# Optimization experiments

Hardware: AMD Instinct MI355X
Metric: run time of the kernel (lower is better)

The kernel has to match this reference:

```python
import jax, jax.numpy as jnp
import numpy as np

EMBED_DIM = 1024
BATCH = 4
SEQ = 2048


def setup_inputs() -> dict:
    key = jax.random.key(0)
    ks = jax.random.split(key, 9)
    D = EMBED_DIM
    s = 1.0 / np.sqrt(D)
    inputs = jax.random.normal(ks[0], (BATCH, SEQ, D), dtype=jnp.float32)
    rotation_params = jax.random.normal(ks[1], (D, D), dtype=jnp.float32) * s
    entangle_params = jax.random.normal(ks[2], (D, D), dtype=jnp.float32) * s
    Wq = jax.random.normal(ks[3], (D, D), dtype=jnp.float32) * s
    bq = jax.random.normal(ks[4], (D,), dtype=jnp.float32) * 0.01
    Wk = jax.random.normal(ks[5], (D, D), dtype=jnp.float32) * s
    bk = jax.random.normal(ks[6], (D,), dtype=jnp.float32) * 0.01
    Wv = jax.random.normal(ks[7], (D, D), dtype=jnp.float32) * s
    bv = jax.random.normal(ks[8], (D,), dtype=jnp.float32) * 0.01
    # causal mask: True = masked out (matches torch masked_fill semantics)
    mask = jnp.triu(jnp.ones((SEQ, SEQ), dtype=bool), k=1)
    return {"inputs": inputs, "rotation_params": rotation_params,
            "entangle_params": entangle_params, "Wq": Wq, "bq": bq,
            "Wk": Wk, "bk": bk, "Wv": Wv, "bv": bv, "mask": mask}


def reference(inputs, rotation_params, entangle_params, Wq, bq, Wk, bk, Wv, bv, mask):
    D = inputs.shape[-1]
    # q = Linear(x) @ R^T ; k = Linear(x) @ E^T ; v = Linear(x)
    q = (jnp.einsum('bsd,ed->bse', inputs, Wq) + bq) @ rotation_params.T
    k = (jnp.einsum('bsd,ed->bse', inputs, Wk) + bk) @ entangle_params.T
    v = jnp.einsum('bsd,ed->bse', inputs, Wv) + bv
    scores = jnp.einsum('bqd,bkd->bqk', q, k) / jnp.sqrt(jnp.float32(D))
    scores = jnp.where(mask, jnp.float32(-jnp.inf), scores)
    probs = jax.nn.softmax(scores, axis=-1)  # dropout=0.0 -> identity
    return jnp.einsum('bqk,bkd->bqd', probs, v)
```

## Files before the change

### kernel.cpp

```cpp
#include <hip/hip_runtime.h>
#include <hip/hip_bf16.h>
#include <stdint.h>
#include <math.h>

#define DD 1024
#define SS 2048
#define BB 4

typedef __bf16 bf16;
typedef __bf16 bf16x8 __attribute__((ext_vector_type(8)));
typedef __bf16 bf16x4 __attribute__((ext_vector_type(4)));
typedef float f32x4 __attribute__((ext_vector_type(4)));

__device__ __forceinline__ void gload_lds16(const bf16* g, bf16* l) {
  __builtin_amdgcn_global_load_lds(
      (const __attribute__((address_space(1))) void*)g,
      (__attribute__((address_space(3))) void*)l, 16, 0, 0);
}

__global__ __launch_bounds__(256) void prep_all(
    const float* __restrict__ x, const float* __restrict__ R,
    const float* __restrict__ E, const float* __restrict__ Wv,
    const float* __restrict__ Wq, const float* __restrict__ Wk,
    const float* __restrict__ bq, const float* __restrict__ bk,
    const float* __restrict__ bv, bf16* __restrict__ xb,
    bf16* __restrict__ Rb, bf16* __restrict__ Eb, bf16* __restrict__ Wvb,
    bf16* __restrict__ WqT, bf16* __restrict__ WkT, float* __restrict__ bias,
    float* __restrict__ rowsums) {
  int bid = blockIdx.x;
  int t = threadIdx.x;
  if (bid < 11264) {
    const float* src;
    bf16* dst;
    int base;
    if (bid < 8192) { src = x; dst = xb; base = bid; }
    else if (bid < 9216) { src = R; dst = Rb; base = bid - 8192; }
    else if (bid < 10240) { src = E; dst = Eb; base = bid - 9216; }
    else { src = Wv; dst = Wvb; base = bid - 10240; }
    int i = (base * 256 + t) * 4;
    float4 v = *(const float4*)(src + i);
    bf16x4 o;
    o.x = (bf16)v.x; o.y = (bf16)v.y; o.z = (bf16)v.z; o.w = (bf16)v.w;
    *(bf16x4*)(dst + i) = o;
  } else if (bid < 13312) {
    int r2 = bid - 11264;
    const float* src = (r2 >= 1024) ? Wk : Wq;
    bf16* dst = (r2 >= 1024) ? WkT : WqT;
    int rem = r2 & 1023;
    int bx = rem & 31, by = rem >> 5;
    __shared__ float tile[32][33];
    int tx = t & 31, ty = t >> 5;
    int xcol = bx * 32 + tx;
    int y0 = by * 32;
    for (int r = ty; r < 32; r += 8)
      tile[r][tx] = src[(y0 + r) * DD + xcol];
    __syncthreads();
    int dx = by * 32 + tx;
    int dy0 = bx * 32;
    for (int r = ty; r < 32; r += 8)
      dst[(dy0 + r) * DD + dx] = (bf16)tile[tx][r];
  } else if (bid < 16384) {
    int e = bid - 13312;
    if (e >= 2048) { if (t == 0) bias[e] = bv[e - 2048]; return; }
    const float* M = (e < 1024) ? R : E;
    const float* bb = (e < 1024) ? bq : bk;
    int row = e & 1023;
    float s = 0.f;
    for (int f = t; f < DD; f += 256) s += M[row * DD + f] * bb[f];
    for (int o = 32; o >= 1; o >>= 1) s += __shfl_xor(s, o, 64);
    __shared__ float red[4];
    if ((t & 63) == 0) red[t >> 6] = s;
    __syncthreads();
    if (t == 0) bias[e] = red[0] + red[1] + red[2] + red[3];
  } else {
    int idx = (bid - 16384) * 256 + t;
    rowsums[idx] = 0.f;
  }
}

#define QSTGA(pa, kt)                                                        \
  gload_lds16(A + (long)(w * 16 + srow) * DD + (kt) * 32 + scg,              \
              As + (pa) * 4096 + w * 512)
#define QSTGB(pb, h, kt)                                                     \
  gload_lds16(B + (long)((h) * 128 + w * 16 + srow) * DD + (kt) * 32 + scg,  \
              Bs + (pb) * 8192 + (h) * 4096 + w * 512)

#define QTILE(pa, pb, pa1, pb2, kA, kB, DOA, DOB, WAITN)                     \
  {                                                                          \
    bf16x8 af[4], bfr[4];                                                    \
    _Pragma("unroll") for (int i_ = 0; i_ < 4; i_++)                         \
        af[i_] = *(const bf16x8*)(a_base + (pa) * 4096 + i_ * 512);          \
    _Pragma("unroll") for (int j_ = 0; j_ < 4; j_++)                         \
        bfr[j_] = *(const bf16x8*)(b_base + (pb) * 8192 + j_ * 512);         \
    if (DOA) { QSTGA(pa1, kA); }                                             \
    if (DOB) { QSTGB(pb2, 0, kB); QSTGB(pb2, 1, kB); }                       \
    __builtin_amdgcn_s_barrier();                                            \
    asm volatile("s_waitcnt lgkmcnt(0)" ::: "memory");                       \
    __builtin_amdgcn_sched_barrier(0);                                       \
    __builtin_amdgcn_s_setprio(1);                                           \
    _Pragma("unroll") for (int i_ = 0; i_ < 4; i_++)                         \
        _Pragma("unroll") for (int j_ = 0; j_ < 4; j_++) acc[i_][j_] =       \
        __builtin_amdgcn_mfma_f32_16x16x32_bf16(af[i_], bfr[j_],             \
                                                acc[i_][j_], 0, 0, 0);       \
    __builtin_amdgcn_s_setprio(0);                                           \
    __builtin_amdgcn_sched_barrier(0);                                       \
    if ((WAITN) == 2) asm volatile("s_waitcnt vmcnt(2)" ::: "memory");       \
    if ((WAITN) == 0) asm volatile("s_waitcnt vmcnt(0)" ::: "memory");       \
    __builtin_amdgcn_s_barrier();                                            \
    __builtin_amdgcn_sched_barrier(0);                                       \
  }

#define QPROLOGUE_AND_LOOP                                                   \
  QSTGA(0, 0);                                                               \
  QSTGB(0, 0, 0); QSTGB(0, 1, 0);                                            \
  QSTGB(1, 0, 1); QSTGB(1, 1, 1);                                            \
  asm volatile("s_waitcnt vmcnt(2)" ::: "memory");                           \
  __builtin_amdgcn_s_barrier();                                              \
  __builtin_amdgcn_sched_barrier(0);                                         \
  _Pragma("unroll 1") for (int t6 = 0; t6 < 30; t6 += 6) {                   \
    QTILE(0, 0, 1, 2, t6 + 1, t6 + 2, 1, 1, 2)                               \
    QTILE(1, 1, 0, 0, t6 + 2, t6 + 3, 1, 1, 2)                               \
    QTILE(0, 2, 1, 1, t6 + 3, t6 + 4, 1, 1, 2)                               \
    QTILE(1, 0, 0, 2, t6 + 4, t6 + 5, 1, 1, 2)                               \
    QTILE(0, 1, 1, 0, t6 + 5, t6 + 6, 1, 1, 2)                               \
    QTILE(1, 2, 0, 1, t6 + 6, t6 + 7, 1, 1, 2)                               \
  }                                                                          \
  QTILE(0, 0, 1, 0, 31, 0, 1, 0, 0)     \
  QTILE(1, 1, 0, 0, 0, 0, 0, 0, -1)

__global__ __launch_bounds__(512, 4) void gemm_qkv(
    const bf16* __restrict__ Ag, const bf16* __restrict__ Bg,
    bf16* __restrict__ Cg, const float* __restrict__ bias,
    bf16* __restrict__ vTp) {
  __shared__ __align__(16) bf16 smem[32768];
  bf16* As = smem;
  bf16* Bs = smem + 8192;

  int id = (int)blockIdx.y * 12 + (int)blockIdx.x;
  int wg = (id & 7) * 96 + (id >> 3);
  int ck = wg / 96, r96 = wg % 96;
  int bx = (ck & 3) * 3 + r96 % 3;
  int by = (ck >> 2) * 32 + r96 / 3;
  long m0 = (long)by * 128, n0 = (long)bx * 256;
  const bf16* A = Ag + m0 * DD;
  const bf16* B = Bg + n0 * DD;

  int t = threadIdx.x;
  int w = t >> 6, l = t & 63;
  int wm = w >> 2, wn = w & 3;
  int ln = l & 15, quad = l >> 4;

  int srow = l >> 2;
  int scg = ((l & 3) ^ ((l >> 3) & 3)) * 8;
  int rdslot = (quad ^ ((ln >> 1) & 3)) * 8;
  const bf16* a_base = As + (wm * 64 + ln) * 32 + rdslot;
  const bf16* b_base = Bs + (wn * 64 + ln) * 32 + rdslot;

  f32x4 acc[4][4];
#pragma unroll
  for (int i = 0; i < 4; i++)
#pragma unroll
    for (int j = 0; j < 4; j++) acc[i][j] = f32x4{0.f, 0.f, 0.f, 0.f};

  QPROLOGUE_AND_LOOP

  __syncthreads();

  if (n0 < 2048) {
    bf16* C = Cg + m0 * 3072 + n0;
#pragma unroll
    for (int i = 0; i < 4; i++) {
      int rb = wm * 64 + i * 16 + quad * 4;
#pragma unroll
      for (int j = 0; j < 4; j++) {
        int col = wn * 64 + j * 16 + ln;
        float bv_ = bias[n0 + col];
#pragma unroll
        for (int r = 0; r < 4; r++)
          C[(long)(rb + r) * 3072 + col] = (bf16)(acc[i][j][r] + bv_);
      }
    }
  } else {
    int d0 = (int)n0 - 2048;
    int b = (int)(m0 >> 11);
    int s0 = (int)(m0 & 2047);
#pragma unroll
    for (int i = 0; i < 4; i++) {
      int sl = wm * 64 + i * 16 + quad * 4;
#pragma unroll
      for (int j = 0; j < 4; j++) {
        int d = wn * 64 + j * 16 + ln;
        float bv_ = bias[n0 + d];
#pragma unroll
        for (int r = 0; r < 4; r++)
          smem[d * 128 + ((sl + r) ^ ((d & 7) << 3))] =
              (bf16)(acc[i][j][r] + bv_);
      }
    }
    __syncthreads();
    int d = t >> 1, sh = t & 1;
    bf16* dst = vTp + (long)b * DD * SS + (long)(d0 + d) * SS + s0 + sh * 64;
#pragma unroll
    for (int c = 0; c < 8; ++c) {
      int sc = (sh * 64 + c * 8) ^ ((d & 7) << 3);
      *(bf16x8*)(dst + c * 8) = *(const bf16x8*)(smem + d * 128 + sc);
    }
  }
}

#define CSTGA(pa, kt)                                                        \
  gload_lds16(Aq + (long)(w * 16 + srow) * 3072 + (kt) * 32 + scg,           \
              As + (pa) * 4096 + w * 512)
#define CSTGB(pb, h, kt)                                                     \
  gload_lds16(Bk + (long)((h) * 128 + w * 16 + srow) * 3072 + (kt) * 32 +    \
                  scg,                                                       \
              Bs + (pb) * 8192 + (h) * 4096 + w * 512)

#define CTILE(pa, pb, pa1, pb2, kA, kB, DOA, DOB, WAITN)                     \
  {                                                                          \
    bf16x8 af[4], bfr[4];                                                    \
    _Pragma("unroll") for (int i_ = 0; i_ < 4; i_++)                         \
        af[i_] = *(const bf16x8*)(a_base + (pa) * 4096 + i_ * 512);          \
    _Pragma("unroll") for (int j_ = 0; j_ < 4; j_++)                         \
        bfr[j_] = *(const bf16x8*)(b_base + (pb) * 8192 + j_ * 512);         \
    if (DOA) { CSTGA(pa1, kA); }                                             \
    if (DOB) { CSTGB(pb2, 0, kB); CSTGB(pb2, 1, kB); }                       \
    __builtin_amdgcn_s_barrier();                                            \
    asm volatile("s_waitcnt lgkmcnt(0)" ::: "memory");                       \
    __builtin_amdgcn_sched_barrier(0);                                       \
    __builtin_amdgcn_s_setprio(1);                                           \
    _Pragma("unroll") for (int i_ = 0; i_ < 4; i_++)                         \
        _Pragma("unroll") for (int j_ = 0; j_ < 4; j_++) acc[i_][j_] =       \
        __builtin_amdgcn_mfma_f32_16x16x32_bf16(af[i_], bfr[j_],             \
                                                acc[i_][j_], 0, 0, 0);       \
    __builtin_amdgcn_s_setprio(0);                                           \
    __builtin_amdgcn_sched_barrier(0);                                       \
    if ((WAITN) == 2) asm volatile("s_waitcnt vmcnt(2)" ::: "memory");       \
    if ((WAITN) == 0) asm volatile("s_waitcnt vmcnt(0)" ::: "memory");       \
    __builtin_amdgcn_s_barrier();                                            \
    __builtin_amdgcn_sched_barrier(0);                                       \
  }

__global__ __launch_bounds__(512, 4) void scores256(
    const bf16* __restrict__ qkvp, bf16* __restrict__ P,
    float* __restrict__ rowsums) {
  __shared__ __align__(16) bf16 smem[32768];
  bf16* As = smem;
  bf16* Bs = smem + 8192;

  int bz = blockIdx.z;
  int id = (int)blockIdx.x;
  int q = (id & 7) * 9 + (id >> 3);
  int s = (int)sqrtf((float)q + 0.5f);
  while (s * s > q) s--;
  while ((s + 1) * (s + 1) <= q) s++;
  int by, bxc;
  if (q >= s * (s + 1)) { by = 2 * s; bxc = q - s * (s + 1); }
  else { by = 2 * s - 1; bxc = q - s * s; }
  long m0 = (long)by * 128, n0 = (long)bxc * 256;
  const bf16* Aq = qkvp + (long)bz * SS * 3072 + m0 * 3072;
  const bf16* Bk = qkvp + 1024 + (long)bz * SS * 3072 + n0 * 3072;

  int t = threadIdx.x;
  int w = t >> 6, l = t & 63;
  int wm = w >> 2, wn = w & 3;
  int ln = l & 15, quad = l >> 4;

  int srow = l >> 2;
  int scg = ((l & 3) ^ ((l >> 3) & 3)) * 8;
  int rdslot = (quad ^ ((ln >> 1) & 3)) * 8;
  const bf16* a_base = As + (wm * 64 + ln) * 32 + rdslot;
  const bf16* b_base = Bs + (wn * 64 + ln) * 32 + rdslot;

  f32x4 acc[4][4];
#pragma unroll
  for (int i = 0; i < 4; i++)
#pragma unroll
    for (int j = 0; j < 4; j++) acc[i][j] = f32x4{0.f, 0.f, 0.f, 0.f};

  CSTGA(0, 0);
  CSTGB(0, 0, 0); CSTGB(0, 1, 0);
  CSTGB(1, 0, 1); CSTGB(1, 1, 1);
  asm volatile("s_waitcnt vmcnt(2)" ::: "memory");
  __builtin_amdgcn_s_barrier();
  __builtin_amdgcn_sched_barrier(0);
#pragma unroll 1
  for (int t6 = 0; t6 < 30; t6 += 6) {
    CTILE(0, 0, 1, 2, t6 + 1, t6 + 2, 1, 1, 2)
    CTILE(1, 1, 0, 0, t6 + 2, t6 + 3, 1, 1, 2)
    CTILE(0, 2, 1, 1, t6 + 3, t6 + 4, 1, 1, 2)
    CTILE(1, 0, 0, 2, t6 + 4, t6 + 5, 1, 1, 2)
    CTILE(0, 1, 1, 0, t6 + 5, t6 + 6, 1, 1, 2)
    CTILE(1, 2, 0, 1, t6 + 6, t6 + 7, 1, 1, 2)
  }
  CTILE(0, 0, 1, 0, 31, 0, 1, 0, 0)
  CTILE(1, 1, 0, 0, 0, 0, 0, 0, -1)

  __syncthreads();

#pragma unroll
  for (int i = 0; i < 4; i++) {
    int rb = wm * 64 + i * 16 + quad * 4;
#pragma unroll
    for (int j = 0; j < 4; j++) {
      int col = wn * 64 + j * 16 + ln;
#pragma unroll
      for (int r = 0; r < 4; r++) {
        int row = rb + r;
        float p = 0.f;
        if (n0 + col <= m0 + row) p = __expf(acc[i][j][r] * 0.03125f);
        smem[row * 256 + (col ^ ((row & 7) << 3))] = (bf16)p;
      }
    }
  }
  __syncthreads();
  int row = t >> 2, qtr = t & 3;
  bf16* Pr = P + (long)bz * SS * SS + (m0 + row) * SS + n0;
  float rsum = 0.f;
#pragma unroll
  for (int c8 = 0; c8 < 8; c8++) {
    int p8 = qtr * 8 + c8;
    int slot = p8 ^ (row & 7);
    bf16x8 v = *(const bf16x8*)(smem + row * 256 + slot * 8);
#pragma unroll
    for (int e = 0; e < 8; e++) rsum += (float)v[e];
    *(bf16x8*)(Pr + p8 * 8) = v;
  }
  rsum += __shfl_xor(rsum, 1, 64);
  rsum += __shfl_xor(rsum, 2, 64);
  if (qtr == 0) atomicAdd(&rowsums[(long)bz * SS + m0 + row], rsum);
}

template <int MODE>
__global__ __launch_bounds__(256, 4)
void gemm_bt(const bf16* __restrict__ Ag, long lda, long sAb,
             const bf16* __restrict__ Bg, long ldb, long sBb,
             void* __restrict__ Cg, long ldc, long sCb,
             const float* __restrict__ bias, float scale, int K,
             bf16* __restrict__ vTp, float* __restrict__ rowsums) {
  __shared__ __align__(16) bf16 smem[16384];
  bf16* As = smem;
  bf16* Bs = smem + 8192;

  int bx = blockIdx.x, by = blockIdx.y, bz = blockIdx.z;
  if (MODE == 0) {
    int nx = (int)gridDim.x;
    int nwg = nx * (int)gridDim.y;
    int id = by * nx + bx;
    int xcd = id & 7, rest = id >> 3;
    int q8 = nwg >> 3, r8 = nwg & 7;
    int wg = (xcd < r8 ? xcd * (q8 + 1) : r8 * (q8 + 1) + (xcd - r8) * q8)
             + rest;
    bx = wg % nx;
    by = wg / nx;
  }
  if (MODE == 2) by = 15 - by;
  long m0 = (long)by * 128, n0 = (long)bx * 128;
  const bf16* A = Ag + (long)bz * sAb + m0 * lda;
  const bf16* Bp = Bg + (long)bz * sBb + n0 * ldb;

  int t = threadIdx.x;
  int w = t >> 6, l = t & 63;
  int lr = l >> 2;
  int lc = (((l & 3) ^ (lr & 3)) * 8);
  int quad = l >> 4, ln = l & 15;
  int wm = w >> 1, wn = w & 1;
  int rdoff = ((quad ^ (ln & 3)) * 8);

  int Keff = (MODE == 2) ? (by + 1) * 128 : K;

  f32x4 acc[4][4];
#pragma unroll
  for (int i = 0; i < 4; i++)
#pragma unroll
    for (int j = 0; j < 4; j++) acc[i][j] = f32x4{0.f, 0.f, 0.f, 0.f};

  const bf16* a_base = As + (wm * 64 + ln) * 32 + rdoff;
  const bf16* b_base = Bs + (wn * 64 + ln) * 32 + rdoff;
  long arow0 = (long)(w * 16 + lr);

#define STG(p, kc0)                                                         \
  {                                                                         \
    int kc = (kc0) + lc;                                                    \
    gload_lds16(A + arow0 * lda + kc, As + (p) * 4096 + w * 512);           \
    gload_lds16(A + (arow0 + 64) * lda + kc,                                \
                As + (p) * 4096 + 2048 + w * 512);                          \
    gload_lds16(Bp + arow0 * ldb + kc, Bs + (p) * 4096 + w * 512);          \
    gload_lds16(Bp + (arow0 + 64) * ldb + kc,                               \
                Bs + (p) * 4096 + 2048 + w * 512);                          \
  }

  STG(0, 0);
  int cur = 0;
  for (int k = 0; k < Keff; k += 32) {
    asm volatile("s_waitcnt vmcnt(0)" ::: "memory");
    __builtin_amdgcn_s_barrier();
    __builtin_amdgcn_sched_barrier(0);
    if (k + 32 < Keff) STG(cur ^ 1, k + 32);
    bf16x8 af[4], bfr[4];
#pragma unroll
    for (int i = 0; i < 4; i++) {
      af[i] = *(const bf16x8*)(a_base + cur * 4096 + i * 512);
      bfr[i] = *(const bf16x8*)(b_base + cur * 4096 + i * 512);
    }
#pragma unroll
    for (int i = 0; i < 4; i++)
#pragma unroll
      for (int j = 0; j < 4; j++)
        acc[i][j] = __builtin_amdgcn_mfma_f32_16x16x32_bf16(
            af[i], bfr[j], acc[i][j], 0, 0, 0);
    cur ^= 1;
  }
#undef STG
  __syncthreads();

  if (MODE == 0) {
    bf16* C = (bf16*)Cg + (long)bz * sCb + m0 * ldc + n0;
#pragma unroll
    for (int i = 0; i < 4; i++) {
      int rb = wm * 64 + i * 16 + quad * 4;
#pragma unroll
      for (int j = 0; j < 4; j++) {
        int col = wn * 64 + j * 16 + ln;
        float bv_ = bias ? bias[n0 + col] : 0.f;
#pragma unroll
        for (int r = 0; r < 4; r++)
          C[(long)(rb + r) * ldc + col] = (bf16)(acc[i][j][r] + bv_);
      }
    }
  } else {
    float* C = (float*)Cg + (long)bz * sCb + m0 * ldc + n0;
    const float* rs = rowsums + (long)bz * SS + m0;
#pragma unroll
    for (int i = 0; i < 4; i++) {
      int rb = wm * 64 + i * 16 + quad * 4;
      float inv[4];
#pragma unroll
      for (int r = 0; r < 4; r++) inv[r] = 1.f / rs[rb + r];
#pragma unroll
      for (int j = 0; j < 4; j++) {
        int col = wn * 64 + j * 16 + ln;
#pragma unroll
        for (int r = 0; r < 4; r++)
          C[(long)(rb + r) * ldc + col] = acc[i][j][r] * inv[r];
      }
    }
  }
}

extern "C" void kernel_launch(void* const* d_in, const int* in_sizes, int n_in,
                              void* d_out, int out_size, void* d_ws,
                              size_t ws_size, hipStream_t stream) {
  const float* x = (const float*)d_in[0];
  const float* R = (const float*)d_in[1];
  const float* E = (const float*)d_in[2];
  const float* Wq = (const float*)d_in[3];
  const float* bq = (const float*)d_in[4];
  const float* Wk = (const float*)d_in[5];
  const float* bk = (const float*)d_in[6];
  const float* Wv = (const float*)d_in[7];
  const float* bv = (const float*)d_in[8];
  float* out = (float*)d_out;

  char* ws = (char*)d_ws;
  bf16* qkv = (bf16*)ws;
  bf16* vT = (bf16*)(ws + 50331648);
  bf16* probs = (bf16*)(ws + 67108864);
  float* rowsums = (float*)(ws + 100663296);
  char* sr = ws + 101711872;
  bf16* xb = (bf16*)sr;
  bf16* Rb = (bf16*)(sr + 16777216);
  bf16* Eb = Rb + 1024 * 1024;
  bf16* WqT = (bf16*)(sr + 20971520);
  bf16* WkT = WqT + 1024 * 1024;
  bf16* wcat = (bf16*)(sr + 25165824);
  float* bias = (float*)(sr + 31457280);

  prep_all<<<16416, 256, 0, stream>>>(x, R, E, Wv, Wq, Wk, bq, bk, bv, xb, Rb,
                                      Eb, wcat + 2048 * DD, WqT, WkT, bias,
                                      rowsums);

  gemm_bt<0><<<dim3(8, 8, 2), 256, 0, stream>>>(
      Rb, DD, 1024 * 1024, WqT, DD, 1024 * 1024, wcat, DD, 1024 * 1024,
      nullptr, 1.f, DD, nullptr, nullptr);

  gemm_qkv<<<dim3(12, 64, 1), 512, 0, stream>>>(xb, wcat, qkv, bias, vT);

  scores256<<<dim3(72, 1, BB), 512, 0, stream>>>(qkv, probs, rowsums);

  gemm_bt<2><<<dim3(8, 16, BB), 256, 0, stream>>>(
      probs, SS, (long)SS * SS, vT, SS, (long)DD * SS, out,
      DD, (long)SS * DD, nullptr, 1.f, SS, nullptr, rowsums);
}
```

Baseline: 290.6 us.

## Replace QKV GEMM with 256x256 tile, 8-phase pipelined kernel using 128KB LDS

Rewrites the fused QKV projection GEMM so each workgroup computes a 256x256 tile instead of 128x256, with BK=64 double-buffered in 128KB of dynamic LDS. The main loop is split into eight MFMA phases that interleave global-to-LDS staging with compute, and the block-to-tile mapping is adjusted for the new grid. The aim is to cut global/LDS traffic per FLOP through larger tile reuse. In exchange, occupancy drops to 2 blocks per CU and register pressure rises with 32 accumulators per wave. The grid becomes 384 tiles, which may leave some CUs with uneven load.

```diff
diff --git a/kernel.cpp b/kernel.cpp
--- a/kernel.cpp
+++ b/kernel.cpp
@@ -78,70 +78,91 @@
   }
 }
 
-#define QSTGA(pa, kt)                                                        \
-  gload_lds16(A + (long)(w * 16 + srow) * DD + (kt) * 32 + scg,              \
-              As + (pa) * 4096 + w * 512)
-#define QSTGB(pb, h, kt)                                                     \
-  gload_lds16(B + (long)((h) * 128 + w * 16 + srow) * DD + (kt) * 32 + scg,  \
-              Bs + (pb) * 8192 + (h) * 4096 + w * 512)
-
-#define QTILE(pa, pb, pa1, pb2, kA, kB, DOA, DOB, WAITN)                     \
+#define AHTO(buf, h) ((buf) * 16384 + (h) * 8192)
+#define BHTO(buf, h) (32768 + (buf) * 16384 + (h) * 8192)
+
+#define STG_A(buf, h, kt)                                                    \
   {                                                                          \
-    bf16x8 af[4], bfr[4];                                                    \
-    _Pragma("unroll") for (int i_ = 0; i_ < 4; i_++)                         \
-        af[i_] = *(const bf16x8*)(a_base + (pa) * 4096 + i_ * 512);          \
-    _Pragma("unroll") for (int j_ = 0; j_ < 4; j_++)                         \
-        bfr[j_] = *(const bf16x8*)(b_base + (pb) * 8192 + j_ * 512);         \
-    if (DOA) { QSTGA(pa1, kA); }                                             \
-    if (DOB) { QSTGB(pb2, 0, kB); QSTGB(pb2, 1, kB); }                       \
-    __builtin_amdgcn_s_barrier();                                            \
-    asm volatile("s_waitcnt lgkmcnt(0)" ::: "memory");                       \
-    __builtin_amdgcn_sched_barrier(0);                                       \
-    __builtin_amdgcn_s_setprio(1);                                           \
-    _Pragma("unroll") for (int i_ = 0; i_ < 4; i_++)                         \
-        _Pragma("unroll") for (int j_ = 0; j_ < 4; j_++) acc[i_][j_] =       \
-        __builtin_amdgcn_mfma_f32_16x16x32_bf16(af[i_], bfr[j_],             \
-                                                acc[i_][j_], 0, 0, 0);       \
-    __builtin_amdgcn_s_setprio(0);                                           \
-    __builtin_amdgcn_sched_barrier(0);                                       \
-    if ((WAITN) == 2) asm volatile("s_waitcnt vmcnt(2)" ::: "memory");       \
-    if ((WAITN) == 0) asm volatile("s_waitcnt vmcnt(0)" ::: "memory");       \
-    __builtin_amdgcn_s_barrier();                                            \
-    __builtin_amdgcn_sched_barrier(0);                                       \
-  }
-
-#define QPROLOGUE_AND_LOOP                                                   \
-  QSTGA(0, 0);                                                               \
-  QSTGB(0, 0, 0); QSTGB(0, 1, 0);                                            \
-  QSTGB(1, 0, 1); QSTGB(1, 1, 1);                                            \
-  asm volatile("s_waitcnt vmcnt(2)" ::: "memory");                           \
+    gload_lds16(A + (long)((h) * 128 + w * 8 + srl) * DD + (kt) * 64 + sch8, \
+                sm + AHTO(buf, h) + w * 512);                                \
+    gload_lds16(                                                             \
+        A + (long)((h) * 128 + 64 + w * 8 + srl) * DD + (kt) * 64 + sch8,    \
+        sm + AHTO(buf, h) + 4096 + w * 512);                                 \
+  }
+#define STG_B(buf, h, kt)                                                    \
+  {                                                                          \
+    gload_lds16(B + (long)((h) * 128 + w * 8 + srl) * DD + (kt) * 64 + sch8, \
+                sm + BHTO(buf, h) + w * 512);                                \
+    gload_lds16(                                                             \
+        B + (long)((h) * 128 + 64 + w * 8 + srl) * DD + (kt) * 64 + sch8,    \
+        sm + BHTO(buf, h) + 4096 + w * 512);                                 \
+  }
+
+#define RDA(buf, ks, dst)                                                    \
+  _Pragma("unroll") for (int mf_ = 0; mf_ < 8; mf_++) dst[mf_] =             \
+      *(const bf16x8*)(sm + ((aoff + (buf) * 16384 + mf_ * 1024) ^           \
+                             ((ks) * 32)));
+#define RDB(buf, ks, dst)                                                    \
+  _Pragma("unroll") for (int nf_ = 0; nf_ < 4; nf_++) dst[nf_] =             \
+      *(const bf16x8*)(sm + ((boff + (buf) * 16384 + nf_ * 1024) ^           \
+                             ((ks) * 32)));
+
+#define MF16(mh, ra_, rb_)                                                   \
+  _Pragma("unroll") for (int mf_ = 0; mf_ < 4; mf_++)                        \
+      _Pragma("unroll") for (int nf_ = 0; nf_ < 4; nf_++)                    \
+          acc[(mh) * 4 + mf_][nf_] =                                         \
+      __builtin_amdgcn_mfma_f32_16x16x32_bf16(ra_[(mh) * 4 + mf_], rb_[nf_], \
+                                              acc[(mh) * 4 + mf_][nf_], 0,  \
+                                              0, 0);
+
+#define PH_OPEN                                                              \
   __builtin_amdgcn_s_barrier();                                              \
+  asm volatile("s_waitcnt lgkmcnt(0)" ::: "memory");                         \
   __builtin_amdgcn_sched_barrier(0);                                         \
-  _Pragma("unroll 1") for (int t6 = 0; t6 < 30; t6 += 6) {                   \
-    QTILE(0, 0, 1, 2, t6 + 1, t6 + 2, 1, 1, 2)                               \
-    QTILE(1, 1, 0, 0, t6 + 2, t6 + 3, 1, 1, 2)                               \
-    QTILE(0, 2, 1, 1, t6 + 3, t6 + 4, 1, 1, 2)                               \
-    QTILE(1, 0, 0, 2, t6 + 4, t6 + 5, 1, 1, 2)                               \
-    QTILE(0, 1, 1, 0, t6 + 5, t6 + 6, 1, 1, 2)                               \
-    QTILE(1, 2, 0, 1, t6 + 6, t6 + 7, 1, 1, 2)                               \
-  }                                                                          \
-  QTILE(0, 0, 1, 0, 31, 0, 1, 0, 0)     \
-  QTILE(1, 1, 0, 0, 0, 0, 0, 0, -1)
-
-__global__ __launch_bounds__(512, 4) void gemm_qkv(
+  __builtin_amdgcn_s_setprio(1);
+#define PH_CLOSE(W)                                                          \
+  __builtin_amdgcn_s_setprio(0);                                             \
+  __builtin_amdgcn_sched_barrier(0);                                         \
+  if ((W) == 4) asm volatile("s_waitcnt vmcnt(4)" ::: "memory");             \
+  if ((W) == 0) asm volatile("s_waitcnt vmcnt(0)" ::: "memory");             \
+  __builtin_amdgcn_s_barrier();                                              \
+  __builtin_amdgcn_sched_barrier(0);
+
+#define ITER8(kt0, DOS, DOT, W4, W8)                                         \
+  {                                                                          \
+    RDA(0, 0, ra0) RDB(0, 0, rb0) STG_B(1, 0, (kt0) + 1);                    \
+    PH_OPEN MF16(0, ra0, rb0) PH_CLOSE(-1)                                   \
+    RDA(0, 1, ra1) RDB(0, 1, rb1) STG_B(1, 1, (kt0) + 1);                    \
+    PH_OPEN MF16(1, ra0, rb0) PH_CLOSE(-1)                                   \
+    if (DOS) STG_A(0, 0, (kt0) + 2);                                         \
+    PH_OPEN MF16(0, ra1, rb1) PH_CLOSE(-1)                                   \
+    if (DOS) STG_A(0, 1, (kt0) + 2);                                         \
+    PH_OPEN MF16(1, ra1, rb1) PH_CLOSE(W4)                                   \
+    RDA(1, 0, ra0) RDB(1, 0, rb0);                                           \
+    if (DOS) STG_B(0, 0, (kt0) + 2);                                         \
+    PH_OPEN MF16(0, ra0, rb0) PH_CLOSE(-1)                                   \
+    RDA(1, 1, ra1) RDB(1, 1, rb1);                                           \
+    if (DOS) STG_B(0, 1, (kt0) + 2);                                         \
+    PH_OPEN MF16(1, ra0, rb0) PH_CLOSE(-1)                                   \
+    if (DOT) STG_A(1, 0, (kt0) + 3);                                         \
+    PH_OPEN MF16(0, ra1, rb1) PH_CLOSE(-1)                                   \
+    if (DOT) STG_A(1, 1, (kt0) + 3);                                         \
+    PH_OPEN MF16(1, ra1, rb1) PH_CLOSE(W8)                                   \
+  }
+
+__global__ __launch_bounds__(512, 2) void gemm256_8ph(
     const bf16* __restrict__ Ag, const bf16* __restrict__ Bg,
     bf16* __restrict__ Cg, const float* __restrict__ bias,
     bf16* __restrict__ vTp) {
-  __shared__ __align__(16) bf16 smem[32768];
-  bf16* As = smem;
-  bf16* Bs = smem + 8192;
+  extern __shared__ __align__(16) char dsm_[];
+  bf16* sm = (bf16*)dsm_;
 
   int id = (int)blockIdx.y * 12 + (int)blockIdx.x;
-  int wg = (id & 7) * 96 + (id >> 3);
-  int ck = wg / 96, r96 = wg % 96;
-  int bx = (ck & 3) * 3 + r96 % 3;
-  int by = (ck >> 2) * 32 + r96 / 3;
-  long m0 = (long)by * 128, n0 = (long)bx * 256;
+  int wg = (id & 7) * 48 + (id >> 3);
+  int ck = wg / 48, r48 = wg % 48;
+  int bx = (ck & 1) * 6 + r48 % 6;
+  int by = (ck >> 1) * 8 + r48 / 6;
+  long m0 = (long)by * 256, n0 = (long)bx * 256;
   const bf16* A = Ag + m0 * DD;
   const bf16* B = Bg + n0 * DD;
 
@@ -150,34 +171,48 @@
   int wm = w >> 2, wn = w & 3;
   int ln = l & 15, quad = l >> 4;
 
-  int srow = l >> 2;
-  int scg = ((l & 3) ^ ((l >> 3) & 3)) * 8;
-  int rdslot = (quad ^ ((ln >> 1) & 3)) * 8;
-  const bf16* a_base = As + (wm * 64 + ln) * 32 + rdslot;
-  const bf16* b_base = Bs + (wn * 64 + ln) * 32 + rdslot;
-
-  f32x4 acc[4][4];
-#pragma unroll
-  for (int i = 0; i < 4; i++)
+  int csw = (quad ^ (ln & 7)) * 8;
+  uint aoff = (uint)(wm * 8192 + ln * 64 + csw);
+  uint boff = (uint)(32768 + (wn >> 1) * 8192 + ((wn & 1) * 64 + ln) * 64 +
+                     csw);
+  int srl = l >> 3;
+  int sch8 = ((l & 7) ^ srl) * 8;
+
+  f32x4 acc[8][4];
+#pragma unroll
+  for (int i = 0; i < 8; i++)
 #pragma unroll
     for (int j = 0; j < 4; j++) acc[i][j] = f32x4{0.f, 0.f, 0.f, 0.f};
-
-  QPROLOGUE_AND_LOOP
+  bf16x8 ra0[8], ra1[8], rb0[4], rb1[4];
+
+  STG_A(0, 0, 0); STG_A(0, 1, 0);
+  STG_B(0, 0, 0); STG_B(0, 1, 0);
+  STG_A(1, 0, 1); STG_A(1, 1, 1);
+  asm volatile("s_waitcnt vmcnt(4)" ::: "memory");
+  __builtin_amdgcn_s_barrier();
+  __builtin_amdgcn_sched_barrier(0);
+
+#pragma unroll 1
+  for (int I = 0; I < 7; ++I) {
+    int kt0 = 2 * I;
+    ITER8(kt0, 1, 1, 4, 4)
+  }
+  ITER8(14, 0, 0, 0, -1)
 
   __syncthreads();
 
   if (n0 < 2048) {
     bf16* C = Cg + m0 * 3072 + n0;
 #pragma unroll
-    for (int i = 0; i < 4; i++) {
-      int rb = wm * 64 + i * 16 + quad * 4;
-#pragma unroll
-      for (int j = 0; j < 4; j++) {
-        int col = wn * 64 + j * 16 + ln;
+    for (int mf = 0; mf < 8; mf++) {
+      int rb = wm * 128 + mf * 16 + quad * 4;
+#pragma unroll
+      for (int nf = 0; nf < 4; nf++) {
+        int col = wn * 64 + nf * 16 + ln;
         float bv_ = bias[n0 + col];
 #pragma unroll
         for (int r = 0; r < 4; r++)
-          C[(long)(rb + r) * 3072 + col] = (bf16)(acc[i][j][r] + bv_);
+          C[(long)(rb + r) * 3072 + col] = (bf16)(acc[mf][nf][r] + bv_);
       }
     }
   } else {
@@ -185,25 +220,25 @@
     int b = (int)(m0 >> 11);
     int s0 = (int)(m0 & 2047);
 #pragma unroll
-    for (int i = 0; i < 4; i++) {
-      int sl = wm * 64 + i * 16 + quad * 4;
-#pragma unroll
-      for (int j = 0; j < 4; j++) {
-        int d = wn * 64 + j * 16 + ln;
+    for (int mf = 0; mf < 8; mf++) {
+      int sl = wm * 128 + mf * 16 + quad * 4;
+#pragma unroll
+      for (int nf = 0; nf < 4; nf++) {
+        int d = wn * 64 + nf * 16 + ln;
         float bv_ = bias[n0 + d];
 #pragma unroll
         for (int r = 0; r < 4; r++)
-          smem[d * 128 + ((sl + r) ^ ((d & 7) << 3))] =
-              (bf16)(acc[i][j][r] + bv_);
+          sm[d * 256 + ((sl + r) ^ ((d & 7) << 3))] =
+              (bf16)(acc[mf][nf][r] + bv_);
       }
     }
     __syncthreads();
     int d = t >> 1, sh = t & 1;
-    bf16* dst = vTp + (long)b * DD * SS + (long)(d0 + d) * SS + s0 + sh * 64;
-#pragma unroll
-    for (int c = 0; c < 8; ++c) {
-      int sc = (sh * 64 + c * 8) ^ ((d & 7) << 3);
-      *(bf16x8*)(dst + c * 8) = *(const bf16x8*)(smem + d * 128 + sc);
+    bf16* dst = vTp + (long)b * DD * SS + (long)(d0 + d) * SS + s0 + sh * 128;
+#pragma unroll
+    for (int c = 0; c < 16; ++c) {
+      int sc = (sh * 128 + c * 8) ^ ((d & 7) << 3);
+      *(bf16x8*)(dst + c * 8) = *(const bf16x8*)(sm + d * 256 + sc);
     }
   }
 }
@@ -476,6 +511,10 @@
   bf16* wcat = (bf16*)(sr + 25165824);
   float* bias = (float*)(sr + 31457280);
 
+  (void)hipFuncSetAttribute(reinterpret_cast<const void*>(gemm256_8ph),
+                            hipFuncAttributeMaxDynamicSharedMemorySize,
+                            131072);
+
   prep_all<<<16416, 256, 0, stream>>>(x, R, E, Wv, Wq, Wk, bq, bk, bv, xb, Rb,
                                       Eb, wcat + 2048 * DD, WqT, WkT, bias,
                                       rowsums);
@@ -484,7 +523,8 @@
       Rb, DD, 1024 * 1024, WqT, DD, 1024 * 1024, wcat, DD, 1024 * 1024,
       nullptr, 1.f, DD, nullptr, nullptr);
 
-  gemm_qkv<<<dim3(12, 64, 1), 512, 0, stream>>>(xb, wcat, qkv, bias, vT);
+  gemm256_8ph<<<dim3(12, 32, 1), 512, 131072, stream>>>(xb, wcat, qkv, bias,
+                                                        vT);
 
   scores256<<<dim3(72, 1, BB), 512, 0, stream>>>(qkv, probs, rowsums);
 
```

New measurement: 320.5 us. 10.3% more time.

## Rewrite QKV GEMM with 128x128 tiles and register double-buffered LDS pipeline

Applied to the files above, without the earlier changes.

Replaces the 128x256-tile, 512-thread QKV projection GEMM with a 128x128-tile, 256-thread kernel. The new kernel prefetches the next k-slice's LDS fragments into a second register set while issuing MFMAs on the current one, and uses a two-stage LDS ring. The grid doubles in x and the XCD-aware block swizzle is rewritten to match. This trades larger per-block reuse for more blocks and a simpler overlap of LDS reads with compute. It also waits on vmcnt(0) every iteration, which may expose global load latency.

```diff
diff --git a/kernel.cpp b/kernel.cpp
--- a/kernel.cpp
+++ b/kernel.cpp
@@ -78,83 +78,70 @@
   }
 }
 
-#define QSTGA(pa, kt)                                                        \
-  gload_lds16(A + (long)(w * 16 + srow) * DD + (kt) * 32 + scg,              \
-              As + (pa) * 4096 + w * 512)
-#define QSTGB(pb, h, kt)                                                     \
-  gload_lds16(B + (long)((h) * 128 + w * 16 + srow) * DD + (kt) * 32 + scg,  \
-              Bs + (pb) * 8192 + (h) * 4096 + w * 512)
-
-#define QTILE(pa, pb, pa1, pb2, kA, kB, DOA, DOB, WAITN)                     \
+#define RPSTG(p, kt)                                                         \
   {                                                                          \
-    bf16x8 af[4], bfr[4];                                                    \
-    _Pragma("unroll") for (int i_ = 0; i_ < 4; i_++)                         \
-        af[i_] = *(const bf16x8*)(a_base + (pa) * 4096 + i_ * 512);          \
-    _Pragma("unroll") for (int j_ = 0; j_ < 4; j_++)                         \
-        bfr[j_] = *(const bf16x8*)(b_base + (pb) * 8192 + j_ * 512);         \
-    if (DOA) { QSTGA(pa1, kA); }                                             \
-    if (DOB) { QSTGB(pb2, 0, kB); QSTGB(pb2, 1, kB); }                       \
-    __builtin_amdgcn_s_barrier();                                            \
+    int kc = (kt) * 32 + lc;                                                 \
+    gload_lds16(A + arow0 * DD + kc, As + (p) * 4096 + w * 512);             \
+    gload_lds16(A + (arow0 + 64) * DD + kc,                                  \
+                As + (p) * 4096 + 2048 + w * 512);                           \
+    gload_lds16(B + arow0 * DD + kc, Bs + (p) * 4096 + w * 512);             \
+    gload_lds16(B + (arow0 + 64) * DD + kc,                                  \
+                Bs + (p) * 4096 + 2048 + w * 512);                           \
+  }
+
+#define RPRD(a_, b_, p)                                                      \
+  _Pragma("unroll") for (int i_ = 0; i_ < 4; i_++) {                         \
+    a_[i_] = *(const bf16x8*)(a_base + (p) * 4096 + i_ * 512);               \
+    b_[i_] = *(const bf16x8*)(b_base + (p) * 4096 + i_ * 512);               \
+  }
+
+#define RPMM(a_, b_)                                                         \
+  _Pragma("unroll") for (int i_ = 0; i_ < 4; i_++)                           \
+      _Pragma("unroll") for (int j_ = 0; j_ < 4; j_++) acc[i_][j_] =         \
+      __builtin_amdgcn_mfma_f32_16x16x32_bf16(a_[i_], b_[j_],                \
+                                              acc[i_][j_], 0, 0, 0);
+
+#define RPITER(aC, bC, aN, bN, t)                                            \
+  {                                                                          \
     asm volatile("s_waitcnt lgkmcnt(0)" ::: "memory");                       \
+    asm volatile("s_waitcnt vmcnt(0)" ::: "memory");                         \
     __builtin_amdgcn_sched_barrier(0);                                       \
-    __builtin_amdgcn_s_setprio(1);                                           \
-    _Pragma("unroll") for (int i_ = 0; i_ < 4; i_++)                         \
-        _Pragma("unroll") for (int j_ = 0; j_ < 4; j_++) acc[i_][j_] =       \
-        __builtin_amdgcn_mfma_f32_16x16x32_bf16(af[i_], bfr[j_],             \
-                                                acc[i_][j_], 0, 0, 0);       \
-    __builtin_amdgcn_s_setprio(0);                                           \
-    __builtin_amdgcn_sched_barrier(0);                                       \
-    if ((WAITN) == 2) asm volatile("s_waitcnt vmcnt(2)" ::: "memory");       \
-    if ((WAITN) == 0) asm volatile("s_waitcnt vmcnt(0)" ::: "memory");       \
     __builtin_amdgcn_s_barrier();                                            \
     __builtin_amdgcn_sched_barrier(0);                                       \
-  }
-
-#define QPROLOGUE_AND_LOOP                                                   \
-  QSTGA(0, 0);                                                               \
-  QSTGB(0, 0, 0); QSTGB(0, 1, 0);                                            \
-  QSTGB(1, 0, 1); QSTGB(1, 1, 1);                                            \
-  asm volatile("s_waitcnt vmcnt(2)" ::: "memory");                           \
-  __builtin_amdgcn_s_barrier();                                              \
-  __builtin_amdgcn_sched_barrier(0);                                         \
-  _Pragma("unroll 1") for (int t6 = 0; t6 < 30; t6 += 6) {                   \
-    QTILE(0, 0, 1, 2, t6 + 1, t6 + 2, 1, 1, 2)                               \
-    QTILE(1, 1, 0, 0, t6 + 2, t6 + 3, 1, 1, 2)                               \
-    QTILE(0, 2, 1, 1, t6 + 3, t6 + 4, 1, 1, 2)                               \
-    QTILE(1, 0, 0, 2, t6 + 4, t6 + 5, 1, 1, 2)                               \
-    QTILE(0, 1, 1, 0, t6 + 5, t6 + 6, 1, 1, 2)                               \
-    QTILE(1, 2, 0, 1, t6 + 6, t6 + 7, 1, 1, 2)                               \
-  }                                                                          \
-  QTILE(0, 0, 1, 0, 31, 0, 1, 0, 0)     \
-  QTILE(1, 1, 0, 0, 0, 0, 0, 0, -1)
-
-__global__ __launch_bounds__(512, 4) void gemm_qkv(
+    RPRD(aN, bN, ((t) + 1) & 1)                                              \
+    RPSTG((t) & 1, (t) + 2)                                                  \
+    RPMM(aC, bC)                                                             \
+  }
+
+__global__ __launch_bounds__(256, 3) void gemm_qkv_rp(
     const bf16* __restrict__ Ag, const bf16* __restrict__ Bg,
     bf16* __restrict__ Cg, const float* __restrict__ bias,
     bf16* __restrict__ vTp) {
-  __shared__ __align__(16) bf16 smem[32768];
+  __shared__ __align__(16) bf16 smem[16384];
   bf16* As = smem;
   bf16* Bs = smem + 8192;
 
-  int id = (int)blockIdx.y * 12 + (int)blockIdx.x;
-  int wg = (id & 7) * 96 + (id >> 3);
-  int ck = wg / 96, r96 = wg % 96;
-  int bx = (ck & 3) * 3 + r96 % 3;
-  int by = (ck >> 2) * 32 + r96 / 3;
-  long m0 = (long)by * 128, n0 = (long)bx * 256;
+  int id = (int)blockIdx.y * 24 + (int)blockIdx.x;
+  int wg = (id & 7) * 192 + (id >> 3);
+  int xcd = wg / 192, r = wg % 192;
+  int bxg = r >> 5, rr = r & 31;
+  int bx = bxg * 4 + (rr & 3);
+  int by = xcd * 8 + (rr >> 2);
+  long m0 = (long)by * 128, n0 = (long)bx * 128;
   const bf16* A = Ag + m0 * DD;
   const bf16* B = Bg + n0 * DD;
 
   int t = threadIdx.x;
   int w = t >> 6, l = t & 63;
-  int wm = w >> 2, wn = w & 3;
-  int ln = l & 15, quad = l >> 4;
-
-  int srow = l >> 2;
-  int scg = ((l & 3) ^ ((l >> 3) & 3)) * 8;
-  int rdslot = (quad ^ ((ln >> 1) & 3)) * 8;
-  const bf16* a_base = As + (wm * 64 + ln) * 32 + rdslot;
-  const bf16* b_base = Bs + (wn * 64 + ln) * 32 + rdslot;
+  int lr = l >> 2;
+  int lc = (((l & 3) ^ (lr & 3)) * 8);
+  int quad = l >> 4, ln = l & 15;
+  int wm = w >> 1, wn = w & 1;
+  int rdoff = ((quad ^ (ln & 3)) * 8);
+  long arow0 = (long)(w * 16 + lr);
+
+  const bf16* a_base = As + (wm * 64 + ln) * 32 + rdoff;
+  const bf16* b_base = Bs + (wn * 64 + ln) * 32 + rdoff;
 
   f32x4 acc[4][4];
 #pragma unroll
@@ -162,7 +149,28 @@
 #pragma unroll
     for (int j = 0; j < 4; j++) acc[i][j] = f32x4{0.f, 0.f, 0.f, 0.f};
 
-  QPROLOGUE_AND_LOOP
+  bf16x8 aA[4], bA[4], aB[4], bB[4];
+
+  RPSTG(0, 0)
+  RPSTG(1, 1)
+  asm volatile("s_waitcnt vmcnt(4)" ::: "memory");
+  __builtin_amdgcn_s_barrier();
+  __builtin_amdgcn_sched_barrier(0);
+  RPRD(aA, bA, 0)
+
+#pragma unroll 1
+  for (int t2 = 0; t2 < 30; t2 += 2) {
+    RPITER(aA, bA, aB, bB, t2)
+    RPITER(aB, bB, aA, bA, t2 + 1)
+  }
+  asm volatile("s_waitcnt lgkmcnt(0)" ::: "memory");
+  asm volatile("s_waitcnt vmcnt(0)" ::: "memory");
+  __builtin_amdgcn_sched_barrier(0);
+  __builtin_amdgcn_s_barrier();
+  __builtin_amdgcn_sched_barrier(0);
+  RPRD(aB, bB, 1)
+  RPMM(aA, bA)
+  RPMM(aB, bB)
 
   __syncthreads();
 
@@ -484,7 +492,7 @@
       Rb, DD, 1024 * 1024, WqT, DD, 1024 * 1024, wcat, DD, 1024 * 1024,
       nullptr, 1.f, DD, nullptr, nullptr);
 
-  gemm_qkv<<<dim3(12, 64, 1), 512, 0, stream>>>(xb, wcat, qkv, bias, vT);
+  gemm_qkv_rp<<<dim3(24, 64, 1), 256, 0, stream>>>(xb, wcat, qkv, bias, vT);
 
   scores256<<<dim3(72, 1, BB), 512, 0, stream>>>(qkv, probs, rowsums);
 
```

Result: no change. 288.1 us (-0.9%).
